# Kernel tuning notes

Hardware: AMD Instinct MI355X
Metric: run time of the kernel (lower is better)

## Reference

```python
import jax, jax.numpy as jnp
import numpy as np

B, S, L = 2, 1024, 1024
DIM_Q, H, K, D_C, D_CQ, R = 2048, 16, 128, 512, 1536, 64


def _rope_tables(length, dim):
    # matches _RoPECache._build_tables: repeat_interleave(2) layout
    inv = 1.0 / (10000.0 ** (jnp.arange(0, dim, 2, dtype=jnp.float32) / dim))
    f = jnp.arange(length, dtype=jnp.float32)[:, None] * inv[None, :]  # [len, dim/2]
    sin = jnp.repeat(jnp.sin(f), 2, axis=-1)
    cos = jnp.repeat(jnp.cos(f), 2, axis=-1)
    return sin, cos


def _rotate_half(x):
    half = x.shape[-1] // 2
    return jnp.concatenate([-x[..., half:], x[..., :half]], axis=-1)


def _apply_rope(x, sin, cos):
    return x * cos + _rotate_half(x) * sin


def setup_inputs() -> dict:
    key = jax.random.key(0)
    ks = jax.random.split(key, 8)
    return {
        "hidden_q": jax.random.normal(ks[0], (B, S, DIM_Q), jnp.float32),
        "kv_c": jax.random.normal(ks[1], (B, L, D_C), jnp.float32),
        "Wq": jax.random.normal(ks[2], (H * K, DIM_Q), jnp.float32) / np.sqrt(DIM_Q).astype(np.float32),
        "w_kc_q": jax.random.normal(ks[3], (H, K, D_CQ), jnp.float32) / np.sqrt(K).astype(np.float32),
        "w_kc_kv": jax.random.normal(ks[4], (H, K, D_C), jnp.float32) / np.sqrt(K).astype(np.float32),
        "W_qr": jax.random.normal(ks[5], (H, D_CQ, R), jnp.float32) / np.float32(np.sqrt(D_CQ) * np.sqrt(R)),
        "W_kr": jax.random.normal(ks[6], (H, D_C, R), jnp.float32) / np.sqrt(D_C).astype(np.float32),
        "Wo": jax.random.normal(ks[7], (DIM_Q, H * K), jnp.float32) / np.sqrt(H * K).astype(np.float32),
    }


def reference(hidden_q, kv_c, Wq, w_kc_q, w_kc_kv, W_qr, W_kr, Wo):
    Bv, Sv, _ = hidden_q.shape
    _, Lv, _ = kv_c.shape
    # latent -> per-head queries, then decompress to d_cq
    q_hk = (hidden_q @ Wq.T).reshape(Bv, Sv, H, K)          # [B,S,H,K]
    q_big = jnp.einsum('bshk,hkq->bshq', q_hk, w_kc_q)      # [B,S,H,d_cq]
    sin_q, cos_q = _rope_tables(Sv, D_CQ)
    q_big = _apply_rope(q_big, sin_q[None, :, None, :], cos_q[None, :, None, :])
    sin_k, cos_k = _rope_tables(Lv, D_C)
    kv_r = _apply_rope(kv_c, sin_k[None], cos_k[None])      # [B,L,d_c]
    # retrieval projections (scale 1/sqrt(r) baked into W_qr)
    q_r = jnp.einsum('bshq,hqr->bhsr', q_big, W_qr)         # [B,H,S,r]
    k_r = jnp.einsum('bld,hdr->bhlr', kv_r, W_kr)           # [B,H,L,r]
    scores = jnp.einsum('bhsr,bhlr->bhsl', q_r, k_r)
    attn = jax.nn.softmax(scores, axis=-1)
    # values are the (RoPE'd) compressed kv shared across heads
    ctx_c = jnp.einsum('bhsl,bld->bhsd', attn, kv_r)        # [B,H,S,d_c]
    # decompress context: w_kc_kv.transpose(1,2) is [H,d_c,K]
    ctx_lat = jnp.einsum('bhsd,hkd->bhsk', ctx_c, w_kc_kv)  # [B,H,S,K]
    ctx = ctx_lat.transpose(0, 2, 1, 3).reshape(Bv, Sv, H * K)
    return ctx @ Wo.T
```

## Files before the change

### kernel.cpp

```cpp
#include <hip/hip_runtime.h>
#include <hip/hip_bf16.h>


typedef __attribute__((ext_vector_type(8))) short short8;
typedef __attribute__((ext_vector_type(4))) float f32x4;

__device__ __forceinline__ unsigned short f2bs(float v){
  __hip_bfloat16 b = __float2bfloat16(v);
  return *reinterpret_cast<unsigned short*>(&b);
}
__device__ __forceinline__ void storeC(float* p, float v){ *p = v; }
__device__ __forceinline__ void storeC(unsigned short* p, float v){ *p = f2bs(v); }

__device__ __forceinline__ void gl_lds16(const void* g, void* l){
  __builtin_amdgcn_global_load_lds(
      (const __attribute__((address_space(1))) unsigned int*)g,
      (__attribute__((address_space(3))) unsigned int*)l, 16, 0, 0);
}

template<int N> __device__ __forceinline__ void wait_vmcnt(){
  if constexpr (N==0)      asm volatile("s_waitcnt vmcnt(0)" ::: "memory");
  else if constexpr (N==3) asm volatile("s_waitcnt vmcnt(3)" ::: "memory");
  else if constexpr (N==4) asm volatile("s_waitcnt vmcnt(4)" ::: "memory");
  else if constexpr (N==6) asm volatile("s_waitcnt vmcnt(6)" ::: "memory");
  else if constexpr (N==8) asm volatile("s_waitcnt vmcnt(8)" ::: "memory");
  else static_assert(N==0, "unsupported vmcnt");
}

__global__ __launch_bounds__(256) void prep_all(
    float4* __restrict__ rq,
    float* __restrict__ sink, float* __restrict__ cosk,
    const float* __restrict__ hidden, unsigned short* __restrict__ hiddenb,
    const float* __restrict__ Wq, unsigned short* __restrict__ Wqb,
    const float* __restrict__ wkckv, unsigned short* __restrict__ wkckvb,
    const float* __restrict__ Wo, unsigned short* __restrict__ Wob)
{
  int blk = blockIdx.x;
  if (blk < 3072){
    int idx = blk*256 + threadIdx.x;
    int s = idx / 768, j = idx - (idx/768)*768;
    int i1 = j >> 1;
    const float cst = -0.011992631f;
    float f1 = (float)s * __expf(cst * (float)i1);
    float f2 = (float)s * __expf(cst * (float)(384 + i1));
    float s1, c1, s2, c2;
    __sincosf(f1, &s1, &c1);
    __sincosf(f2, &s2, &c2);
    rq[idx] = make_float4(c1, s1, c2, s2);
    return;
  }
  if (blk < 4096){
    int idx = (blk-3072)*256 + threadIdx.x;
    int l = idx >> 8, j = idx & 255;
    const float cst = -0.035977892f;
    float f = (float)l * __expf(cst * (float)j);
    float sv, cv; __sincosf(f, &sv, &cv);
    int base = l*512 + 2*j;
    sink[base] = sv; sink[base+1] = sv;
    cosk[base] = cv; cosk[base+1] = cv;
    return;
  }
  const float* in; unsigned short* out; int i;
  if (blk < 8192){ in = hidden; out = hiddenb; i = (blk-4096)*256 + threadIdx.x; }
  else if (blk < 12288){ in = Wq; out = Wqb; i = (blk-8192)*256 + threadIdx.x; }
  else if (blk < 13312){ in = wkckv; out = wkckvb; i = (blk-12288)*256 + threadIdx.x; }
  else { in = Wo; out = Wob; i = (blk-13313+1)*256 + threadIdx.x; }
  float4 v = *(const float4*)(in + (long)i*4);
  ushort4 u; u.x=f2bs(v.x); u.y=f2bs(v.y); u.z=f2bs(v.z); u.w=f2bs(v.w);
  *(ushort4*)(out + (long)i*4) = u;
}

__global__ __launch_bounds__(256) void transpose_cvt(
    const float* __restrict__ in, unsigned short* __restrict__ out,
    int R, int Cn, long sIn, long sOut)
{
  __shared__ float tile[32][33];
  const float* ip = in + (long)blockIdx.z*sIn;
  unsigned short* op = out + (long)blockIdx.z*sOut;
  int c0 = blockIdx.x*32, r0 = blockIdx.y*32;
  int tr = threadIdx.x>>5, tc = threadIdx.x&31;
  #pragma unroll
  for (int i=0;i<4;i++)
    tile[tr+i*8][tc] = ip[(long)(r0+tr+i*8)*Cn + c0+tc];
  __syncthreads();
  #pragma unroll
  for (int i=0;i<4;i++)
    op[(long)(c0+tr+i*8)*R + r0+tc] = f2bs(tile[tc][tr+i*8]);
}

template<int BM,int BN,int WM,int WN,typename TC>
__global__ __launch_bounds__(256) void gemm_mfma(
    const unsigned short* __restrict__ A, const unsigned short* __restrict__ B,
    TC* __restrict__ C,
    int Kd, int lda, int ldb, int ldc, int Hb,
    long sAb, long sAh, long sBb, long sBh, long sCb, long sCh)
{
  constexpr int MF = WM/16, NF = WN/16;
  constexpr int WGM = BM/WM;
  constexpr int AOPS = (4*BM)/256;
  constexpr int BOPS = (4*BN)/256;
  constexpr int STG  = AOPS + BOPS;

  const int z = blockIdx.z, bb = z/Hb, hh = z - bb*Hb;
  const unsigned short* Ap = A + bb*sAb + hh*sAh;
  const unsigned short* Bp = B + bb*sBb + hh*sBh;
  TC* Cp = C + bb*sCb + hh*sCh;
  const int m0 = blockIdx.x*BM, n0 = blockIdx.y*BN;
  const int t = threadIdx.x, w = t>>6, l = t&63;
  const int wm0 = (w % WGM)*WM, wn0 = (w / WGM)*WN;
  const int lq = l>>4, lm = l&15;

  __shared__ __align__(16) unsigned short As[4][4*BM*8];
  __shared__ __align__(16) unsigned short Bs[4][4*BN*8];

  f32x4 acc[MF][NF];
  #pragma unroll
  for (int mf=0; mf<MF; ++mf)
    #pragma unroll
    for (int nf=0; nf<NF; ++nf)
      acc[mf][nf] = f32x4{0.f,0.f,0.f,0.f};

  auto stage = [&](int buf, int k0){
    #pragma unroll
    for (int o = 0; o < AOPS; ++o){
      int g = o*256 + t;
      int row = g & (BM-1), kq = g / BM;
      gl_lds16(Ap + (long)(m0+row)*lda + k0 + kq*8, &As[buf][(o*256 + w*64)*8]);
    }
    #pragma unroll
    for (int o = 0; o < BOPS; ++o){
      int g = o*256 + t;
      int row = g & (BN-1), kq = g / BN;
      gl_lds16(Bp + (long)(n0+row)*ldb + k0 + kq*8, &Bs[buf][(o*256 + w*64)*8]);
    }
  };

  const int nIter = Kd >> 5;
  stage(0, 0);
  if (1 < nIter) stage(1, 32);
  if (2 < nIter) stage(2, 64);

  for (int it = 0; it < nIter; ++it){
    const int cur = it & 3;
    const int rem = nIter - it;
    if (rem >= 3)      wait_vmcnt<2*STG>();
    else if (rem == 2) wait_vmcnt<STG>();
    else               wait_vmcnt<0>();
    __builtin_amdgcn_s_barrier();

    short8 af[MF], bfr[NF];
    #pragma unroll
    for (int mf=0; mf<MF; ++mf)
      af[mf] = *(const short8*)&As[cur][(lq*BM + wm0 + mf*16 + lm)*8];
    #pragma unroll
    for (int nf=0; nf<NF; ++nf)
      bfr[nf] = *(const short8*)&Bs[cur][(lq*BN + wn0 + nf*16 + lm)*8];
    #pragma unroll
    for (int mf=0; mf<MF; ++mf)
      #pragma unroll
      for (int nf=0; nf<NF; ++nf)
        acc[mf][nf] = __builtin_amdgcn_mfma_f32_16x16x32_bf16(
            af[mf], bfr[nf], acc[mf][nf], 0, 0, 0);

    if (it+3 < nIter) stage((it+3) & 3, (it+3)*32);
  }

  #pragma unroll
  for (int mf=0; mf<MF; ++mf){
    #pragma unroll
    for (int nf=0; nf<NF; ++nf){
      int row = m0 + wm0 + mf*16 + lq*4;
      int col = n0 + wn0 + nf*16 + lm;
      #pragma unroll
      for (int r=0; r<4; ++r)
        storeC(&Cp[(long)(row+r)*ldc + col], acc[mf][nf][r]);
    }
  }
}

__global__ __launch_bounds__(256) void q_fused(
    const unsigned short* __restrict__ A,
    const unsigned short* __restrict__ W1t,
    const unsigned short* __restrict__ W2t,
    const float4* __restrict__ rq,
    unsigned short* __restrict__ qrOut)
{
  const int z = blockIdx.z, bb = z>>4, hh = z&15;
  const int m0 = blockIdx.x*64;
  const unsigned short* Ap = A + (long)bb*2097152 + hh*128;
  const unsigned short* W1 = W1t + (long)hh*196608;
  const unsigned short* W2 = W2t + (long)hh*98304;
  unsigned short* qo = qrOut + ((long)z*1024 + m0)*64;

  const int t = threadIdx.x, w = t>>6, l = t&63;
  const int lq = l>>4, lm = l&15;

  __shared__ __align__(16) unsigned short As[16*64*8];
  __shared__ __align__(16) unsigned short W1s[2][16*64*8];
  __shared__ __align__(16) unsigned short W2s[2][8*64*8];
  __shared__ __align__(16) unsigned short Ps[64*72];

  #pragma unroll
  for (int o=0;o<4;++o){
    int g=o*256+t; int row=g&63, kq=g>>6;
    gl_lds16(Ap + (long)(m0+row)*2048 + kq*8, &As[(o*256+w*64)*8]);
  }
  auto stageW = [&](int buf, int cn){
    #pragma unroll
    for (int o=0;o<4;++o){
      int g=o*256+t; int row=g&63, kq=g>>6;
      int grow = (row<32) ? (cn*32+row) : (736+cn*32+row);
      gl_lds16(W1 + (long)grow*128 + kq*8, &W1s[buf][(o*256+w*64)*8]);
    }
    #pragma unroll
    for (int o=0;o<2;++o){
      int g=o*256+t; int n=g&63, kq=g>>6;
      int qk = (kq<4) ? (cn*32+kq*8) : (736+cn*32+kq*8);
      gl_lds16(W2 + (long)n*1536 + qk, &W2s[buf][(o*256+w*64)*8]);
    }
  };
  stageW(0, 0);
  __syncthreads();

  short8 af[4];
  #pragma unroll
  for (int ks=0; ks<4; ++ks)
    af[ks] = *(const short8*)&As[((ks*4+lq)*64 + w*16 + lm)*8];

  f32x4 accr[4];
  #pragma unroll
  for (int nf=0; nf<4; ++nf) accr[nf] = f32x4{0.f,0.f,0.f,0.f};

  for (int cn = 0; cn < 24; ++cn){
    const int cur = cn & 1;
    if (cn < 23) stageW(cur^1, cn+1);

    f32x4 sa[4];
    #pragma unroll
    for (int nf=0; nf<4; ++nf) sa[nf] = f32x4{0.f,0.f,0.f,0.f};
    #pragma unroll
    for (int ks=0; ks<4; ++ks)
      #pragma unroll
      for (int nf=0; nf<4; ++nf){
        short8 bf = *(const short8*)&W1s[cur][((ks*4+lq)*64 + nf*16 + lm)*8];
        sa[nf] = __builtin_amdgcn_mfma_f32_16x16x32_bf16(af[ks], bf, sa[nf], 0,0,0);
      }

    #pragma unroll
    for (int nf=0; nf<2; ++nf)
      #pragma unroll
      for (int r=0; r<4; ++r){
        int srow = m0 + w*16 + lq*4 + r;
        int j = cn*32 + nf*16 + lm;
        float4 rc = rq[(long)srow*768 + j];
        float xl = sa[nf][r], xh = sa[nf+2][r];
        Ps[(w*16 + lq*4 + r)*72 + nf*16 + lm]      = f2bs(xl*rc.x - xh*rc.y);
        Ps[(w*16 + lq*4 + r)*72 + 32 + nf*16 + lm] = f2bs(xh*rc.z + xl*rc.w);
      }

    #pragma unroll
    for (int ks=0; ks<2; ++ks){
      short8 ap = *(const short8*)&Ps[(w*16 + lm)*72 + ks*32 + lq*8];
      #pragma unroll
      for (int nf=0; nf<4; ++nf){
        short8 bw = *(const short8*)&W2s[cur][((ks*4+lq)*64 + nf*16 + lm)*8];
        accr[nf] = __builtin_amdgcn_mfma_f32_16x16x32_bf16(ap, bw, accr[nf], 0,0,0);
      }
    }
    __syncthreads();
  }

  #pragma unroll
  for (int nf=0; nf<4; ++nf)
    #pragma unroll
    for (int r=0; r<4; ++r)
      qo[(long)(w*16 + lq*4 + r)*64 + nf*16 + lm] = f2bs(accr[nf][r]);
}

__global__ __launch_bounds__(256) void rope_k_kernel(
    const float* __restrict__ kc,
    const float* __restrict__ sk, const float* __restrict__ ck,
    unsigned short* __restrict__ kvrb)
{
  int idx = blockIdx.x*256 + threadIdx.x;
  int row = idx >> 8;
  int d = idx & 255;
  int l = row & 1023;
  long base = (long)row*512;
  float xl = kc[base+d], xh = kc[base+d+256];
  int tb = l*512 + d;
  kvrb[base+d]     = f2bs(xl*ck[tb]     - xh*sk[tb]);
  kvrb[base+d+256] = f2bs(xh*ck[tb+256] + xl*sk[tb+256]);
}

__global__ __launch_bounds__(256) void flash_mfma(
    const unsigned short* __restrict__ qr, const unsigned short* __restrict__ kr,
    const unsigned short* __restrict__ vt, unsigned short* __restrict__ ctx)
{
  const int b = blockIdx.z, h = blockIdx.y, s0 = blockIdx.x*64;
  const int t = threadIdx.x, w = t>>6, l = t&63;
  const int lq = l>>4, lm = l&15;

  __shared__ __align__(16) unsigned short Qs[8*64*8];
  __shared__ __align__(16) unsigned short Ks[2][8*64*8];
  __shared__ __align__(16) unsigned short Vts[2][8*128*8];
  __shared__ __align__(16) unsigned short Ps[64*72];

  const unsigned short* qbase = qr + ((long)(b*16+h)*1024 + s0)*64;
  const unsigned short* kbase = kr + (long)(b*16+h)*65536;
  const unsigned short* vbase = vt + (long)(b*16+h)*131072;

  auto stageKV = [&](int buf, int l0){
    #pragma unroll
    for (int o = 0; o < 2; ++o){
      int g = o*256 + t;
      int row = g & 63, kq = g >> 6;
      gl_lds16(kbase + (long)(l0+row)*64 + kq*8, &Ks[buf][(o*256 + w*64)*8]);
    }
    #pragma unroll
    for (int o = 0; o < 4; ++o){
      int g = o*256 + t;
      int row = g & 127, kq = g >> 7;
      gl_lds16(vbase + (long)row*1024 + l0 + kq*8, &Vts[buf][(o*256 + w*64)*8]);
    }
  };

  #pragma unroll
  for (int o = 0; o < 2; ++o){
    int g = o*256 + t;
    int row = g & 63, kq = g >> 6;
    gl_lds16(qbase + (long)row*64 + kq*8, &Qs[(o*256 + w*64)*8]);
  }
  stageKV(0, 0);
  __syncthreads();
  short8 aq[2];
  #pragma unroll
  for (int ks = 0; ks < 2; ++ks)
    aq[ks] = *(const short8*)&Qs[((ks*4+lq)*64 + w*16 + lm)*8];

  float m_run[4], l_run[4];
  #pragma unroll
  for (int r = 0; r < 4; ++r){ m_run[r] = -3e38f; l_run[r] = 0.f; }
  f32x4 acc_o[8];
  #pragma unroll
  for (int nf = 0; nf < 8; ++nf) acc_o[nf] = f32x4{0.f,0.f,0.f,0.f};

  for (int it = 0; it < 16; ++it){
    const int cur = it & 1;
    __syncthreads();
    if (it < 15) stageKV(cur^1, (it+1)*64);

    f32x4 acc_s[4];
    #pragma unroll
    for (int nf = 0; nf < 4; ++nf) acc_s[nf] = f32x4{0.f,0.f,0.f,0.f};
    #pragma unroll
    for (int ks = 0; ks < 2; ++ks)
      #pragma unroll
      for (int nf = 0; nf < 4; ++nf){
        short8 bf = *(const short8*)&Ks[cur][((ks*4+lq)*64 + nf*16 + lm)*8];
        acc_s[nf] = __builtin_amdgcn_mfma_f32_16x16x32_bf16(
            aq[ks], bf, acc_s[nf], 0, 0, 0);
      }

    float tmax[4];
    #pragma unroll
    for (int r = 0; r < 4; ++r)
      tmax[r] = fmaxf(fmaxf(acc_s[0][r], acc_s[1][r]),
                      fmaxf(acc_s[2][r], acc_s[3][r]));
    #pragma unroll
    for (int mask = 1; mask < 16; mask <<= 1)
      #pragma unroll
      for (int r = 0; r < 4; ++r)
        tmax[r] = fmaxf(tmax[r], __shfl_xor(tmax[r], mask));
    float alpha[4], rsum[4];
    #pragma unroll
    for (int r = 0; r < 4; ++r){
      float mnew = fmaxf(m_run[r], tmax[r]);
      alpha[r] = __expf(m_run[r] - mnew);
      m_run[r] = mnew;
      rsum[r] = 0.f;
    }
    #pragma unroll
    for (int nf = 0; nf < 4; ++nf)
      #pragma unroll
      for (int r = 0; r < 4; ++r){
        float p = __expf(acc_s[nf][r] - m_run[r]);
        rsum[r] += p;
        Ps[(w*16 + lq*4 + r)*72 + nf*16 + lm] = f2bs(p);
      }
    #pragma unroll
    for (int mask = 1; mask < 16; mask <<= 1)
      #pragma unroll
      for (int r = 0; r < 4; ++r)
        rsum[r] += __shfl_xor(rsum[r], mask);
    #pragma unroll
    for (int r = 0; r < 4; ++r)
      l_run[r] = l_run[r]*alpha[r] + rsum[r];

    #pragma unroll
    for (int nf = 0; nf < 8; ++nf)
      #pragma unroll
      for (int r = 0; r < 4; ++r)
        acc_o[nf][r] *= alpha[r];

    short8 ap[2];
    #pragma unroll
    for (int ks = 0; ks < 2; ++ks)
      ap[ks] = *(const short8*)&Ps[(w*16 + lm)*72 + ks*32 + lq*8];
    #pragma unroll
    for (int ks = 0; ks < 2; ++ks)
      #pragma unroll
      for (int nf = 0; nf < 8; ++nf){
        short8 bv = *(const short8*)&Vts[cur][((ks*4+lq)*128 + nf*16 + lm)*8];
        acc_o[nf] = __builtin_amdgcn_mfma_f32_16x16x32_bf16(
            ap[ks], bv, acc_o[nf], 0, 0, 0);
      }
  }

  float inv[4];
  #pragma unroll
  for (int r = 0; r < 4; ++r) inv[r] = 1.f / l_run[r];
  #pragma unroll
  for (int nf = 0; nf < 8; ++nf)
    #pragma unroll
    for (int r = 0; r < 4; ++r){
      long row = (long)b*1024 + s0 + w*16 + lq*4 + r;
      ctx[row*2048 + h*128 + nf*16 + lm] = f2bs(acc_o[nf][r]*inv[r]);
    }
}

extern "C" void kernel_launch(void* const* d_in, const int* in_sizes, int n_in,
                              void* d_out, int out_size, void* d_ws, size_t ws_size,
                              hipStream_t stream)
{
  const float* hidden_q = (const float*)d_in[0];
  const float* kv_c     = (const float*)d_in[1];
  const float* Wq       = (const float*)d_in[2];
  const float* w_kc_q   = (const float*)d_in[3];
  const float* w_kc_kv  = (const float*)d_in[4];
  const float* W_qr     = (const float*)d_in[5];
  const float* W_kr     = (const float*)d_in[6];
  const float* Wo       = (const float*)d_in[7];
  float* out = (float*)d_out;

  char* wsb = (char*)d_ws;
  size_t off = 0;
  auto take = [&](size_t bytes)->void*{
    void* p = wsb + off; off += (bytes + 255) & ~(size_t)255; return p;
  };
  unsigned short* q_rb  = (unsigned short*)take(4194304);
  unsigned short* k_rb  = (unsigned short*)take(4194304);
  unsigned short* kv_rb = (unsigned short*)take(2097152);
  float* sink   = (float*)take(2097152);
  float* cosk   = (float*)take(2097152);
  float4* ropeq4 = (float4*)take(12582912);
  unsigned short* q_hk   = (unsigned short*)take(8388608);
  unsigned short* wkcqT  = (unsigned short*)take(6291456);
  unsigned short* WqrT   = (unsigned short*)take(3145728);
  unsigned short* wkckvb = (unsigned short*)take(2097152);
  unsigned short* WkrT   = (unsigned short*)take(1048576);
  unsigned short* Vt     = (unsigned short*)take(8388608);
  unsigned short* hiddenb = (unsigned short*)take(8388608);
  unsigned short* Wqb     = (unsigned short*)take(8388608);
  unsigned short* Wob     = (unsigned short*)take(8388608);
  unsigned short* ctx_lat = (unsigned short*)take(8388608);

  prep_all<<<17408, 256, 0, stream>>>(ropeq4, sink, cosk,
      hidden_q, hiddenb, Wq, Wqb, w_kc_kv, wkckvb, Wo, Wob);
  transpose_cvt<<<dim3(48,4,16), 256, 0, stream>>>(w_kc_q, wkcqT, 128, 1536, 196608, 196608);
  transpose_cvt<<<dim3(2,48,16), 256, 0, stream>>>(W_qr, WqrT, 1536, 64, 98304, 98304);
  transpose_cvt<<<dim3(2,16,16), 256, 0, stream>>>(W_kr, WkrT, 512, 64, 32768, 32768);

  gemm_mfma<128,128,64,64,unsigned short><<<dim3(16,16,1),256,0,stream>>>(
      hiddenb, Wqb, q_hk, 2048, 2048,2048,2048, 1, 0,0, 0,0, 0,0);

  q_fused<<<dim3(16,1,32),256,0,stream>>>(q_hk, wkcqT, WqrT, ropeq4, q_rb);

  rope_k_kernel<<<2048, 256, 0, stream>>>(kv_c, sink, cosk, kv_rb);

  gemm_mfma<128,64,64,32,unsigned short><<<dim3(8,1,32),256,0,stream>>>(
      kv_rb, WkrT, k_rb, 512, 512,512,64, 16,
      524288,0, 0,32768, 1048576,65536);

  gemm_mfma<128,128,64,64,unsigned short><<<dim3(1,8,32),256,0,stream>>>(
      wkckvb, kv_rb, Vt, 512, 512,512,1024, 16,
      0,65536, 524288,0, 2097152,131072);

  flash_mfma<<<dim3(16,16,2),256,0,stream>>>(q_rb, k_rb, Vt, ctx_lat);

  gemm_mfma<128,128,64,64,float><<<dim3(16,16,1),256,0,stream>>>(
      ctx_lat, Wob, out, 2048, 2048,2048,2048, 1, 0,0, 0,0, 0,0);
}
```

Baseline: 345.6 us.

## Double q_fused row tile, prefetch RoPE tables, use vmcnt-based barriers

q_fused now processes 128 rows per block instead of 64, so each staged W1/W2 chunk is reused by two M-fragments per wave and the grid halves. RoPE cos/sin values are loaded into registers before issuing the next weight stage, and __syncthreads is replaced by partial s_waitcnt vmcnt plus raw s_barrier. This lets prefetches for the next chunk stay in flight. The flash kernel gets the same partial-wait barrier scheme. Also fixes a harmless index expression in prep_all. Risks: larger register and LDS use, fewer blocks (256) for occupancy, and correctness depends on the hand-counted vmcnt values.

```diff
diff --git a/kernel.cpp b/kernel.cpp
--- a/kernel.cpp
+++ b/kernel.cpp
@@ -19,11 +19,14 @@
 }
 
 template<int N> __device__ __forceinline__ void wait_vmcnt(){
-  if constexpr (N==0)      asm volatile("s_waitcnt vmcnt(0)" ::: "memory");
-  else if constexpr (N==3) asm volatile("s_waitcnt vmcnt(3)" ::: "memory");
-  else if constexpr (N==4) asm volatile("s_waitcnt vmcnt(4)" ::: "memory");
-  else if constexpr (N==6) asm volatile("s_waitcnt vmcnt(6)" ::: "memory");
-  else if constexpr (N==8) asm volatile("s_waitcnt vmcnt(8)" ::: "memory");
+  if constexpr (N==0)       asm volatile("s_waitcnt vmcnt(0)" ::: "memory");
+  else if constexpr (N==3)  asm volatile("s_waitcnt vmcnt(3)" ::: "memory");
+  else if constexpr (N==4)  asm volatile("s_waitcnt vmcnt(4)" ::: "memory");
+  else if constexpr (N==6)  asm volatile("s_waitcnt vmcnt(6)" ::: "memory");
+  else if constexpr (N==8)  asm volatile("s_waitcnt vmcnt(8)" ::: "memory");
+  else if constexpr (N==14) asm volatile("s_waitcnt vmcnt(14)" ::: "memory");
+  else if constexpr (N==16) asm volatile("s_waitcnt vmcnt(16)" ::: "memory");
+  else if constexpr (N==22) asm volatile("s_waitcnt vmcnt(22)" ::: "memory");
   else static_assert(N==0, "unsupported vmcnt");
 }
 
@@ -64,7 +67,7 @@
   if (blk < 8192){ in = hidden; out = hiddenb; i = (blk-4096)*256 + threadIdx.x; }
   else if (blk < 12288){ in = Wq; out = Wqb; i = (blk-8192)*256 + threadIdx.x; }
   else if (blk < 13312){ in = wkckv; out = wkckvb; i = (blk-12288)*256 + threadIdx.x; }
-  else { in = Wo; out = Wob; i = (blk-13313+1)*256 + threadIdx.x; }
+  else { in = Wo; out = Wob; i = (blk-13312)*256 + threadIdx.x; }
   float4 v = *(const float4*)(in + (long)i*4);
   ushort4 u; u.x=f2bs(v.x); u.y=f2bs(v.y); u.z=f2bs(v.z); u.w=f2bs(v.w);
   *(ushort4*)(out + (long)i*4) = u;
@@ -186,7 +189,7 @@
     unsigned short* __restrict__ qrOut)
 {
   const int z = blockIdx.z, bb = z>>4, hh = z&15;
-  const int m0 = blockIdx.x*64;
+  const int m0 = blockIdx.x*128;
   const unsigned short* Ap = A + (long)bb*2097152 + hh*128;
   const unsigned short* W1 = W1t + (long)hh*196608;
   const unsigned short* W2 = W2t + (long)hh*98304;
@@ -195,14 +198,14 @@
   const int t = threadIdx.x, w = t>>6, l = t&63;
   const int lq = l>>4, lm = l&15;
 
-  __shared__ __align__(16) unsigned short As[16*64*8];
+  __shared__ __align__(16) unsigned short As[16*128*8];
   __shared__ __align__(16) unsigned short W1s[2][16*64*8];
   __shared__ __align__(16) unsigned short W2s[2][8*64*8];
-  __shared__ __align__(16) unsigned short Ps[64*72];
-
-  #pragma unroll
-  for (int o=0;o<4;++o){
-    int g=o*256+t; int row=g&63, kq=g>>6;
+  __shared__ __align__(16) unsigned short Ps[128*72];
+
+  #pragma unroll
+  for (int o=0;o<8;++o){
+    int g=o*256+t; int row=g&127, kq=g>>7;
     gl_lds16(Ap + (long)(m0+row)*2048 + kq*8, &As[(o*256+w*64)*8]);
   }
   auto stageW = [&](int buf, int cn){
@@ -222,59 +225,84 @@
   stageW(0, 0);
   __syncthreads();
 
-  short8 af[4];
-  #pragma unroll
-  for (int ks=0; ks<4; ++ks)
-    af[ks] = *(const short8*)&As[((ks*4+lq)*64 + w*16 + lm)*8];
-
-  f32x4 accr[4];
-  #pragma unroll
-  for (int nf=0; nf<4; ++nf) accr[nf] = f32x4{0.f,0.f,0.f,0.f};
+  short8 af[2][4];
+  #pragma unroll
+  for (int mf=0; mf<2; ++mf)
+    #pragma unroll
+    for (int ks=0; ks<4; ++ks)
+      af[mf][ks] = *(const short8*)&As[((ks*4+lq)*128 + w*32 + mf*16 + lm)*8];
+
+  f32x4 accr[2][4];
+  #pragma unroll
+  for (int mf=0; mf<2; ++mf)
+    #pragma unroll
+    for (int nf=0; nf<4; ++nf) accr[mf][nf] = f32x4{0.f,0.f,0.f,0.f};
 
   for (int cn = 0; cn < 24; ++cn){
     const int cur = cn & 1;
+
+    float4 rc_reg[2][2][4];
+    #pragma unroll
+    for (int mf=0; mf<2; ++mf)
+      #pragma unroll
+      for (int nf=0; nf<2; ++nf)
+        #pragma unroll
+        for (int r=0; r<4; ++r){
+          int srow = m0 + w*32 + mf*16 + lq*4 + r;
+          rc_reg[mf][nf][r] = rq[(long)srow*768 + cn*32 + nf*16 + lm];
+        }
     if (cn < 23) stageW(cur^1, cn+1);
-
-    f32x4 sa[4];
-    #pragma unroll
-    for (int nf=0; nf<4; ++nf) sa[nf] = f32x4{0.f,0.f,0.f,0.f};
+    if (cn < 23) wait_vmcnt<22>(); else wait_vmcnt<16>();
+    __builtin_amdgcn_s_barrier();
+
+    f32x4 sa[2][4];
+    #pragma unroll
+    for (int mf=0; mf<2; ++mf)
+      #pragma unroll
+      for (int nf=0; nf<4; ++nf) sa[mf][nf] = f32x4{0.f,0.f,0.f,0.f};
     #pragma unroll
     for (int ks=0; ks<4; ++ks)
       #pragma unroll
       for (int nf=0; nf<4; ++nf){
         short8 bf = *(const short8*)&W1s[cur][((ks*4+lq)*64 + nf*16 + lm)*8];
-        sa[nf] = __builtin_amdgcn_mfma_f32_16x16x32_bf16(af[ks], bf, sa[nf], 0,0,0);
+        sa[0][nf] = __builtin_amdgcn_mfma_f32_16x16x32_bf16(af[0][ks], bf, sa[0][nf], 0,0,0);
+        sa[1][nf] = __builtin_amdgcn_mfma_f32_16x16x32_bf16(af[1][ks], bf, sa[1][nf], 0,0,0);
       }
 
     #pragma unroll
-    for (int nf=0; nf<2; ++nf)
-      #pragma unroll
-      for (int r=0; r<4; ++r){
-        int srow = m0 + w*16 + lq*4 + r;
-        int j = cn*32 + nf*16 + lm;
-        float4 rc = rq[(long)srow*768 + j];
-        float xl = sa[nf][r], xh = sa[nf+2][r];
-        Ps[(w*16 + lq*4 + r)*72 + nf*16 + lm]      = f2bs(xl*rc.x - xh*rc.y);
-        Ps[(w*16 + lq*4 + r)*72 + 32 + nf*16 + lm] = f2bs(xh*rc.z + xl*rc.w);
-      }
+    for (int mf=0; mf<2; ++mf)
+      #pragma unroll
+      for (int nf=0; nf<2; ++nf)
+        #pragma unroll
+        for (int r=0; r<4; ++r){
+          int prow = w*32 + mf*16 + lq*4 + r;
+          float4 rc = rc_reg[mf][nf][r];
+          float xl = sa[mf][nf][r], xh = sa[mf][nf+2][r];
+          Ps[prow*72 + nf*16 + lm]      = f2bs(xl*rc.x - xh*rc.y);
+          Ps[prow*72 + 32 + nf*16 + lm] = f2bs(xh*rc.z + xl*rc.w);
+        }
 
     #pragma unroll
     for (int ks=0; ks<2; ++ks){
-      short8 ap = *(const short8*)&Ps[(w*16 + lm)*72 + ks*32 + lq*8];
+      short8 ap0 = *(const short8*)&Ps[(w*32 + lm)*72 + ks*32 + lq*8];
+      short8 ap1 = *(const short8*)&Ps[(w*32 + 16 + lm)*72 + ks*32 + lq*8];
       #pragma unroll
       for (int nf=0; nf<4; ++nf){
         short8 bw = *(const short8*)&W2s[cur][((ks*4+lq)*64 + nf*16 + lm)*8];
-        accr[nf] = __builtin_amdgcn_mfma_f32_16x16x32_bf16(ap, bw, accr[nf], 0,0,0);
+        accr[0][nf] = __builtin_amdgcn_mfma_f32_16x16x32_bf16(ap0, bw, accr[0][nf], 0,0,0);
+        accr[1][nf] = __builtin_amdgcn_mfma_f32_16x16x32_bf16(ap1, bw, accr[1][nf], 0,0,0);
       }
     }
-    __syncthreads();
-  }
-
-  #pragma unroll
-  for (int nf=0; nf<4; ++nf)
-    #pragma unroll
-    for (int r=0; r<4; ++r)
-      qo[(long)(w*16 + lq*4 + r)*64 + nf*16 + lm] = f2bs(accr[nf][r]);
+    __builtin_amdgcn_s_barrier();
+  }
+
+  #pragma unroll
+  for (int mf=0; mf<2; ++mf)
+    #pragma unroll
+    for (int nf=0; nf<4; ++nf)
+      #pragma unroll
+      for (int r=0; r<4; ++r)
+        qo[(long)(w*32 + mf*16 + lq*4 + r)*64 + nf*16 + lm] = f2bs(accr[mf][nf][r]);
 }
 
 __global__ __launch_bounds__(256) void rope_k_kernel(
@@ -347,8 +375,9 @@
 
   for (int it = 0; it < 16; ++it){
     const int cur = it & 1;
-    __syncthreads();
-    if (it < 15) stageKV(cur^1, (it+1)*64);
+    if (it < 15){ stageKV(cur^1, (it+1)*64); wait_vmcnt<6>(); }
+    else        { wait_vmcnt<0>(); }
+    __builtin_amdgcn_s_barrier();
 
     f32x4 acc_s[4];
     #pragma unroll
@@ -415,6 +444,7 @@
         acc_o[nf] = __builtin_amdgcn_mfma_f32_16x16x32_bf16(
             ap[ks], bv, acc_o[nf], 0, 0, 0);
       }
+    __builtin_amdgcn_s_barrier();
   }
 
   float inv[4];
@@ -474,7 +504,7 @@
   gemm_mfma<128,128,64,64,unsigned short><<<dim3(16,16,1),256,0,stream>>>(
       hiddenb, Wqb, q_hk, 2048, 2048,2048,2048, 1, 0,0, 0,0, 0,0);
 
-  q_fused<<<dim3(16,1,32),256,0,stream>>>(q_hk, wkcqT, WqrT, ropeq4, q_rb);
+  q_fused<<<dim3(8,1,32),256,0,stream>>>(q_hk, wkcqT, WqrT, ropeq4, q_rb);
 
   rope_k_kernel<<<2048, 256, 0, stream>>>(kv_c, sink, cosk, kv_rb);
 
```

Result: slower. 354.6 us (+2.6%).

## Replace full syncthreads with partial vmcnt waits and raw barriers in pipelines

Applied to the files above, without the earlier changes.

In the q-projection and attention loops, `__syncthreads` (which drains every outstanding load) is replaced by explicit `s_waitcnt vmcnt(N)` plus `s_barrier`. This lets the next stage's global-to-LDS prefetch stay in flight while the current buffer is consumed. The RoPE table values are also loaded into registers ahead of the prefetch so their latency overlaps with it. A Wo conversion index expression is simplified without changing its value. The counts are hand-chosen and risk reading LDS before the data lands if they are wrong.

```diff
diff --git a/kernel.cpp b/kernel.cpp
--- a/kernel.cpp
+++ b/kernel.cpp
@@ -19,11 +19,14 @@
 }
 
 template<int N> __device__ __forceinline__ void wait_vmcnt(){
-  if constexpr (N==0)      asm volatile("s_waitcnt vmcnt(0)" ::: "memory");
-  else if constexpr (N==3) asm volatile("s_waitcnt vmcnt(3)" ::: "memory");
-  else if constexpr (N==4) asm volatile("s_waitcnt vmcnt(4)" ::: "memory");
-  else if constexpr (N==6) asm volatile("s_waitcnt vmcnt(6)" ::: "memory");
-  else if constexpr (N==8) asm volatile("s_waitcnt vmcnt(8)" ::: "memory");
+  if constexpr (N==0)       asm volatile("s_waitcnt vmcnt(0)" ::: "memory");
+  else if constexpr (N==3)  asm volatile("s_waitcnt vmcnt(3)" ::: "memory");
+  else if constexpr (N==4)  asm volatile("s_waitcnt vmcnt(4)" ::: "memory");
+  else if constexpr (N==6)  asm volatile("s_waitcnt vmcnt(6)" ::: "memory");
+  else if constexpr (N==8)  asm volatile("s_waitcnt vmcnt(8)" ::: "memory");
+  else if constexpr (N==14) asm volatile("s_waitcnt vmcnt(14)" ::: "memory");
+  else if constexpr (N==16) asm volatile("s_waitcnt vmcnt(16)" ::: "memory");
+  else if constexpr (N==22) asm volatile("s_waitcnt vmcnt(22)" ::: "memory");
   else static_assert(N==0, "unsupported vmcnt");
 }
 
@@ -64,7 +67,7 @@
   if (blk < 8192){ in = hidden; out = hiddenb; i = (blk-4096)*256 + threadIdx.x; }
   else if (blk < 12288){ in = Wq; out = Wqb; i = (blk-8192)*256 + threadIdx.x; }
   else if (blk < 13312){ in = wkckv; out = wkckvb; i = (blk-12288)*256 + threadIdx.x; }
-  else { in = Wo; out = Wob; i = (blk-13313+1)*256 + threadIdx.x; }
+  else { in = Wo; out = Wob; i = (blk-13312)*256 + threadIdx.x; }
   float4 v = *(const float4*)(in + (long)i*4);
   ushort4 u; u.x=f2bs(v.x); u.y=f2bs(v.y); u.z=f2bs(v.z); u.w=f2bs(v.w);
   *(ushort4*)(out + (long)i*4) = u;
@@ -233,7 +236,18 @@
 
   for (int cn = 0; cn < 24; ++cn){
     const int cur = cn & 1;
+
+    float4 rc_reg[2][4];
+    #pragma unroll
+    for (int nf=0; nf<2; ++nf)
+      #pragma unroll
+      for (int r=0; r<4; ++r){
+        int srow = m0 + w*16 + lq*4 + r;
+        rc_reg[nf][r] = rq[(long)srow*768 + cn*32 + nf*16 + lm];
+      }
     if (cn < 23) stageW(cur^1, cn+1);
+    if (cn < 23) wait_vmcnt<14>(); else wait_vmcnt<8>();
+    __builtin_amdgcn_s_barrier();
 
     f32x4 sa[4];
     #pragma unroll
@@ -250,12 +264,11 @@
     for (int nf=0; nf<2; ++nf)
       #pragma unroll
       for (int r=0; r<4; ++r){
-        int srow = m0 + w*16 + lq*4 + r;
-        int j = cn*32 + nf*16 + lm;
-        float4 rc = rq[(long)srow*768 + j];
+        int prow = w*16 + lq*4 + r;
+        float4 rc = rc_reg[nf][r];
         float xl = sa[nf][r], xh = sa[nf+2][r];
-        Ps[(w*16 + lq*4 + r)*72 + nf*16 + lm]      = f2bs(xl*rc.x - xh*rc.y);
-        Ps[(w*16 + lq*4 + r)*72 + 32 + nf*16 + lm] = f2bs(xh*rc.z + xl*rc.w);
+        Ps[prow*72 + nf*16 + lm]      = f2bs(xl*rc.x - xh*rc.y);
+        Ps[prow*72 + 32 + nf*16 + lm] = f2bs(xh*rc.z + xl*rc.w);
       }
 
     #pragma unroll
@@ -267,7 +280,7 @@
         accr[nf] = __builtin_amdgcn_mfma_f32_16x16x32_bf16(ap, bw, accr[nf], 0,0,0);
       }
     }
-    __syncthreads();
+    __builtin_amdgcn_s_barrier();
   }
 
   #pragma unroll
@@ -347,8 +360,9 @@
 
   for (int it = 0; it < 16; ++it){
     const int cur = it & 1;
-    __syncthreads();
-    if (it < 15) stageKV(cur^1, (it+1)*64);
+    if (it < 15){ stageKV(cur^1, (it+1)*64); wait_vmcnt<6>(); }
+    else        { wait_vmcnt<0>(); }
+    __builtin_amdgcn_s_barrier();
 
     f32x4 acc_s[4];
     #pragma unroll
@@ -415,6 +429,7 @@
         acc_o[nf] = __builtin_amdgcn_mfma_f32_16x16x32_bf16(
             ap[ks], bv, acc_o[nf], 0, 0, 0);
       }
+    __builtin_amdgcn_s_barrier();
   }
 
   float inv[4];
```

After: 343.5 us. No clear change (-0.6%).
